# Optimization experiments

Measured on AMD Instinct MI355X. Metric: run time of the kernel, lower is better.

The kernel has to match this reference:

```python
import jax, jax.numpy as jnp
import numpy as np

G, IN_DIM, OUT_DIM = 100000, 256, 128
B, N = 4096, 8192
ALPHA = 0.2          # LeakyReLU negative slope
NEG_INF = -9e15      # same masking constant as the torch module
EPS = 1e-12          # F.normalize eps


def setup_inputs() -> dict:
    key = jax.random.key(0)
    k1, k2, k3, k4, k5, k6, k7 = jax.random.split(key, 7)
    global_feature = jax.random.normal(k1, (G, IN_DIM), dtype=jnp.float32)
    nodes = jax.random.randint(k2, (B,), 0, G, dtype=jnp.int32)
    unique_nodes = jax.random.randint(k3, (N,), 0, G, dtype=jnp.int32)
    mask = jax.random.randint(k4, (B, N), 0, 2, dtype=jnp.int32)
    # ensure every row has at least one neighbor (original always includes self)
    mask = mask.at[:, 0].set(1)
    # xavier_uniform with gain=1.414
    gain = 1.414
    lim_W = gain * np.sqrt(6.0 / (IN_DIM + OUT_DIM))
    W = jax.random.uniform(k5, (IN_DIM, OUT_DIM), jnp.float32, -lim_W, lim_W)
    lim_a = gain * np.sqrt(6.0 / (2 * OUT_DIM + 1))
    a1 = jax.random.uniform(k6, (OUT_DIM,), jnp.float32, -lim_a, lim_a)
    a2 = jax.random.uniform(k7, (OUT_DIM,), jnp.float32, -lim_a, lim_a)
    return {"global_feature": global_feature, "nodes": nodes,
            "unique_nodes": unique_nodes, "mask": mask,
            "W": W, "a1": a1, "a2": a2}


def reference(global_feature, nodes, unique_nodes, mask, W, a1, a2):
    # project gathered features: [B,F], [N,F]
    h_nodes = global_feature[nodes] @ W
    h_neigh = global_feature[unique_nodes] @ W
    # additive attention scores; equivalent to cat([h_i,h_j]) @ a
    e = h_nodes @ a1[:, None] + (h_neigh @ a2)[None, :]   # [B,N]
    e = jnp.where(e >= 0, e, ALPHA * e)                    # leaky relu
    e = jnp.where(mask > 0, e, NEG_INF)
    attention = jax.nn.softmax(e, axis=1)                  # [B,N]
    out = attention @ h_neigh                              # [B,F]
    norm = jnp.linalg.norm(out, axis=1, keepdims=True)
    out = out / jnp.maximum(norm, EPS)                     # F.normalize p=2
    return out
```

## Files before the change

### kernel.cpp

```cpp
#include <hip/hip_runtime.h>

#define IN_DIM  256
#define OUT_DIM 128
#define B_ROWS  4096
#define N_COLS  8192
#define ALPHA   0.2f

typedef unsigned short u16;
typedef unsigned int   u32;
typedef __attribute__((ext_vector_type(8))) short short8;
typedef __attribute__((ext_vector_type(4))) float floatx4;

__device__ __forceinline__ float bf2f(u16 v){ return __uint_as_float(((u32)v) << 16); }
__device__ __forceinline__ float bflo(u32 v){ return __uint_as_float(v << 16); }
__device__ __forceinline__ float bfhi(u32 v){ return __uint_as_float(v & 0xffff0000u); }
__device__ __forceinline__ u16 f2bf(float f){
    u32 u = __float_as_uint(f);
    u += 0x7fffu + ((u >> 16) & 1u);
    return (u16)(u >> 16);
}

__global__ __launch_bounds__(256) void k_detect(const u32* __restrict__ g, int* __restrict__ flag){
    __shared__ int votes[256];
    int t = threadIdx.x;
    u32 u = g[t];
    int e = (u >> 7) & 0xFF;
    votes[t] = (e >= 110 && e <= 140) ? 1 : 0;
    __syncthreads();
    for (int s = 128; s > 0; s >>= 1){
        if (t < s) votes[t] += votes[t + s];
        __syncthreads();
    }
    if (t == 0) flag[0] = (votes[0] >= 128) ? 1 : 0;
}

__global__ __launch_bounds__(256) void k_wa(const void* __restrict__ W, const void* __restrict__ a1,
                                            const int* __restrict__ flag, float* __restrict__ Wa1){
    __shared__ float a1s[OUT_DIM];
    int t = threadIdx.x;
    const int isbf = *flag;
    if (t < OUT_DIM) a1s[t] = isbf ? bf2f(((const u16*)a1)[t]) : ((const float*)a1)[t];
    __syncthreads();
    float s = 0.f;
    if (isbf){
        const u32* wr = (const u32*)W + t * (OUT_DIM/2);
#pragma unroll 8
        for (int i = 0; i < OUT_DIM/2; i++){
            u32 g = wr[i];
            s += bflo(g) * a1s[2*i] + bfhi(g) * a1s[2*i+1];
        }
    } else {
        const float* wr = (const float*)W + t * OUT_DIM;
#pragma unroll 8
        for (int c = 0; c < OUT_DIM; c++) s += wr[c] * a1s[c];
    }
    Wa1[t] = s;
}

__global__ __launch_bounds__(128) void k_wb(const void* __restrict__ W, const void* __restrict__ a2,
                                            const int* __restrict__ flag,
                                            u16* __restrict__ WB, float* __restrict__ a2f){
    const int c  = threadIdx.x;
    const int kb = blockIdx.x;
    const int isbf = *flag;
    short8 v;
#pragma unroll
    for (int j = 0; j < 8; j++){
        float w = isbf ? bf2f(((const u16*)W)[(kb*8 + j) * OUT_DIM + c])
                       : ((const float*)W)[(kb*8 + j) * OUT_DIM + c];
        v[j] = (short)f2bf(w);
    }
    ((short8*)WB)[kb * OUT_DIM + c] = v;
    if (kb == 0) a2f[c] = isbf ? bf2f(((const u16*)a2)[c]) : ((const float*)a2)[c];
}

__global__ __launch_bounds__(256) void k_hneigh(const void* __restrict__ gf, const int* __restrict__ uniq,
                                                const u16* __restrict__ WB, const float* __restrict__ a2f,
                                                const int* __restrict__ flag,
                                                u16* __restrict__ hB, float* __restrict__ s_neigh){
    const int n0   = blockIdx.x * 16;
    const int t    = threadIdx.x;
    const int lane = t & 63;
    const int wv   = t >> 6;
    const int q    = lane >> 4;
    const int m    = lane & 15;
    const int isbf = *flag;
    const int jb0  = wv * 2;

    const size_t row = (size_t)uniq[n0 + m];
    const short8* wb8 = (const short8*)WB;

    floatx4 acc0 = {0.f,0.f,0.f,0.f};
    floatx4 acc1 = {0.f,0.f,0.f,0.f};

#pragma unroll
    for (int ks = 0; ks < IN_DIM/32; ks++){
        short8 afrag;
        if (isbf){
            afrag = *(const short8*)((const u16*)gf + row * IN_DIM + ks*32 + q*8);
        } else {
            const float* gp = (const float*)gf + row * IN_DIM + ks*32 + q*8;
            float4 f0 = *(const float4*)gp;
            float4 f1 = *(const float4*)(gp + 4);
            afrag[0] = (short)f2bf(f0.x); afrag[1] = (short)f2bf(f0.y);
            afrag[2] = (short)f2bf(f0.z); afrag[3] = (short)f2bf(f0.w);
            afrag[4] = (short)f2bf(f1.x); afrag[5] = (short)f2bf(f1.y);
            afrag[6] = (short)f2bf(f1.z); afrag[7] = (short)f2bf(f1.w);
        }
        const int kb = ks*4 + q;
        short8 b0 = wb8[kb * OUT_DIM + jb0*16 + m];
        short8 b1 = wb8[kb * OUT_DIM + (jb0+1)*16 + m];
        acc0 = __builtin_amdgcn_mfma_f32_16x16x32_bf16(afrag, b0, acc0, 0, 0, 0);
        acc1 = __builtin_amdgcn_mfma_f32_16x16x32_bf16(afrag, b1, acc1, 0, 0, 0);
    }

    {
        u32 lo0 = (u32)f2bf(acc0[0]) | ((u32)f2bf(acc0[1]) << 16);
        u32 hi0 = (u32)f2bf(acc0[2]) | ((u32)f2bf(acc0[3]) << 16);
        u32 lo1 = (u32)f2bf(acc1[0]) | ((u32)f2bf(acc1[1]) << 16);
        u32 hi1 = (u32)f2bf(acc1[2]) | ((u32)f2bf(acc1[3]) << 16);
        uint2 v0; v0.x = lo0; v0.y = hi0;
        uint2 v1; v1.x = lo1; v1.y = hi1;
        u16* base = hB + (size_t)(n0/8 + (q>>1)) * 1024 + (q&1)*4;
        *(uint2*)(base + (jb0*16 + m) * 8)     = v0;
        *(uint2*)(base + ((jb0+1)*16 + m) * 8) = v1;
    }

    __shared__ float sred[4][16];
    float a2c0 = a2f[jb0*16 + m], a2c1 = a2f[(jb0+1)*16 + m];
#pragma unroll
    for (int reg = 0; reg < 4; reg++){
        float pr = acc0[reg]*a2c0 + acc1[reg]*a2c1;
        pr += __shfl_xor(pr, 1); pr += __shfl_xor(pr, 2);
        pr += __shfl_xor(pr, 4); pr += __shfl_xor(pr, 8);
        if (m == 0) sred[wv][q*4 + reg] = pr;
    }
    __syncthreads();
    if (t < 16) s_neigh[n0 + t] = sred[0][t] + sred[1][t] + sred[2][t] + sred[3][t];
}

__global__ __launch_bounds__(256) void k_snode(const void* __restrict__ gf, const int* __restrict__ nodes,
                                               const float* __restrict__ Wa1, const int* __restrict__ flag,
                                               float* __restrict__ s_node){
    int lane = threadIdx.x & 63, wv = threadIdx.x >> 6;
    int b = blockIdx.x * 4 + wv;
    const int isbf = *flag;
    float4 wa = ((const float4*)Wa1)[lane];
    float x0, x1, x2, x3;
    if (isbf){
        uint2 gg = ((const uint2*)((const u16*)gf + (size_t)nodes[b] * IN_DIM))[lane];
        x0 = bflo(gg.x); x1 = bfhi(gg.x); x2 = bflo(gg.y); x3 = bfhi(gg.y);
    } else {
        float4 gg = ((const float4*)((const float*)gf + (size_t)nodes[b] * IN_DIM))[lane];
        x0 = gg.x; x1 = gg.y; x2 = gg.z; x3 = gg.w;
    }
    float s = x0*wa.x + x1*wa.y + x2*wa.z + x3*wa.w;
    for (int off = 32; off > 0; off >>= 1) s += __shfl_down(s, off);
    if (lane == 0) s_node[b] = s;
}

__global__ __launch_bounds__(512, 2) void k_attn(const int* __restrict__ mask,
                                                 const float* __restrict__ s_node,
                                                 const float* __restrict__ s_neigh,
                                                 const u16* __restrict__ hB,
                                                 const int* __restrict__ flag,
                                                 void* __restrict__ out){
    const int b0   = blockIdx.x * 16;
    const int t    = threadIdx.x;
    const int lane = t & 63;
    const int wv   = t >> 6;
    const int q    = lane >> 4;
    const int m    = lane & 15;

    const int n0   = wv * (N_COLS/8);
    const int KS   = (N_COLS/8) / 32;

    floatx4 acc[8];
#pragma unroll
    for (int jb = 0; jb < 8; jb++){ floatx4 z = {0.f,0.f,0.f,0.f}; acc[jb] = z; }

    const float sn = s_node[b0 + m];
    const int rowoff = (b0 + m) * N_COLS;
    const short8* hb8 = (const short8*)hB;

    for (int ks = 0; ks < KS; ks++){
        const int nb = n0 + ks*32 + q*8;
        int4   ma = *(const int4*)  (mask    + rowoff + nb);
        int4   mb = *(const int4*)  (mask    + rowoff + nb + 4);
        float4 sa = *(const float4*)(s_neigh + nb);
        float4 sb = *(const float4*)(s_neigh + nb + 4);

        float e[8] = { sn+sa.x, sn+sa.y, sn+sa.z, sn+sa.w,
                       sn+sb.x, sn+sb.y, sn+sb.z, sn+sb.w };
        int mk[8] = { ma.x, ma.y, ma.z, ma.w, mb.x, mb.y, mb.z, mb.w };
        short8 afrag;
#pragma unroll
        for (int j = 0; j < 8; j++){
            float ee = fmaxf(e[j], ALPHA*e[j]);
            ee = fminf(ee, 60.f);
            float p = mk[j] > 0 ? __expf(ee) : 0.f;
            afrag[j] = (short)f2bf(p);
        }

        const int kb = ((n0 + ks*32) >> 3) + q;
#pragma unroll
        for (int jb = 0; jb < 8; jb++){
            short8 bfr = hb8[kb * OUT_DIM + jb*16 + m];
            acc[jb] = __builtin_amdgcn_mfma_f32_16x16x32_bf16(afrag, bfr, acc[jb], 0, 0, 0);
        }
    }

    __shared__ float red[8][16][128];
#pragma unroll
    for (int jb = 0; jb < 8; jb++)
#pragma unroll
        for (int reg = 0; reg < 4; reg++)
            red[wv][q*4 + reg][jb*16 + m] = acc[jb][reg];
    __syncthreads();

    const int c  = t & 127;
    const int rp = t >> 7;
    const int half = (t >> 6) & 1;

    float v[4];
#pragma unroll
    for (int i = 0; i < 4; i++){
        const int r = rp*4 + i;
        float s = 0.f;
#pragma unroll
        for (int w = 0; w < 8; w++) s += red[w][r][c];
        v[i] = s;
    }

    __shared__ float rs[16][2];
#pragma unroll
    for (int i = 0; i < 4; i++){
        float p = v[i] * v[i];
        p += __shfl_xor(p, 1);  p += __shfl_xor(p, 2);  p += __shfl_xor(p, 4);
        p += __shfl_xor(p, 8);  p += __shfl_xor(p, 16); p += __shfl_xor(p, 32);
        if (lane == 0) rs[rp*4 + i][half] = p;
    }
    __syncthreads();

    const int isbf = *flag;
#pragma unroll
    for (int i = 0; i < 4; i++){
        const int r = rp*4 + i;
        float tot = rs[r][0] + rs[r][1];
        float scale = 1.f / fmaxf(sqrtf(tot), 1e-12f);
        float o = v[i] * scale;
        size_t idx = (size_t)(b0 + r) * OUT_DIM + c;
        if (isbf) ((u16*)out)[idx] = f2bf(o);
        else      ((float*)out)[idx] = o;
    }
}

extern "C" void kernel_launch(void* const* d_in, const int* in_sizes, int n_in,
                              void* d_out, int out_size, void* d_ws, size_t ws_size,
                              hipStream_t stream){
    const void* gf    = d_in[0];
    const int*  nodes = (const int*)d_in[1];
    const int*  uniq  = (const int*)d_in[2];
    const int*  mask  = (const int*)d_in[3];
    const void* W     = d_in[4];
    const void* a1    = d_in[5];
    const void* a2    = d_in[6];

    char* ws = (char*)d_ws;
    u16*   hB      = (u16*)ws;
    u16*   WB      = (u16*)(ws + (2u<<20));
    float* s_neigh = (float*)(ws + (2u<<20) + (64u<<10));
    float* s_node  = (float*)(ws + (2u<<20) + (96u<<10));
    float* Wa1     = (float*)(ws + (2u<<20) + (112u<<10));
    float* a2f     = (float*)(ws + (2u<<20) + (113u<<10));
    int*   flag    = (int*)  (ws + (2u<<20) + (114u<<10));

    hipLaunchKernelGGL(k_detect, dim3(1),           dim3(256), 0, stream, (const u32*)gf, flag);
    hipLaunchKernelGGL(k_wa,     dim3(1),           dim3(256), 0, stream, W, a1, flag, Wa1);
    hipLaunchKernelGGL(k_wb,     dim3(32),          dim3(128), 0, stream, W, a2, flag, WB, a2f);
    hipLaunchKernelGGL(k_snode,  dim3(B_ROWS/4),    dim3(256), 0, stream, gf, nodes, Wa1, flag, s_node);
    hipLaunchKernelGGL(k_hneigh, dim3(N_COLS/16),   dim3(256), 0, stream, gf, uniq, WB, a2f, flag, hB, s_neigh);
    hipLaunchKernelGGL(k_attn,   dim3(B_ROWS/16),   dim3(512), 0, stream, mask, s_node, s_neigh, hB, flag, d_out);
}
```

Baseline: 314.7 us.

## Restructure attention into split-N tiles with 32-row reuse and fused prep

Merges the dtype-detect, Wa1, W-repack and node-score kernels into fewer launches, with each wave detecting dtype through ballots. The attention kernel now handles 32 rows per block, so each hB fragment feeds two MFMAs. It splits N across four blocks so the grid grows from 256 to 512 blocks. Probabilities are staged through LDS so mask loads are coalesced along N. Partial sums are merged with LDS atomics, written to a workspace and reduced in a separate normalize kernel, which adds an extra pass and a launch.

```diff
diff --git a/kernel.cpp b/kernel.cpp
--- a/kernel.cpp
+++ b/kernel.cpp
@@ -5,6 +5,7 @@
 #define B_ROWS  4096
 #define N_COLS  8192
 #define ALPHA   0.2f
+#define NSP     4
 
 typedef unsigned short u16;
 typedef unsigned int   u32;
@@ -20,63 +21,51 @@
     return (u16)(u >> 16);
 }
 
-__global__ __launch_bounds__(256) void k_detect(const u32* __restrict__ g, int* __restrict__ flag){
-    __shared__ int votes[256];
-    int t = threadIdx.x;
-    u32 u = g[t];
-    int e = (u >> 7) & 0xFF;
-    votes[t] = (e >= 110 && e <= 140) ? 1 : 0;
-    __syncthreads();
-    for (int s = 128; s > 0; s >>= 1){
-        if (t < s) votes[t] += votes[t + s];
-        __syncthreads();
-    }
-    if (t == 0) flag[0] = (votes[0] >= 128) ? 1 : 0;
-}
-
-__global__ __launch_bounds__(256) void k_wa(const void* __restrict__ W, const void* __restrict__ a1,
-                                            const int* __restrict__ flag, float* __restrict__ Wa1){
-    __shared__ float a1s[OUT_DIM];
-    int t = threadIdx.x;
-    const int isbf = *flag;
-    if (t < OUT_DIM) a1s[t] = isbf ? bf2f(((const u16*)a1)[t]) : ((const float*)a1)[t];
-    __syncthreads();
-    float s = 0.f;
-    if (isbf){
-        const u32* wr = (const u32*)W + t * (OUT_DIM/2);
-#pragma unroll 8
-        for (int i = 0; i < OUT_DIM/2; i++){
-            u32 g = wr[i];
-            s += bflo(g) * a1s[2*i] + bfhi(g) * a1s[2*i+1];
-        }
-    } else {
-        const float* wr = (const float*)W + t * OUT_DIM;
-#pragma unroll 8
-        for (int c = 0; c < OUT_DIM; c++) s += wr[c] * a1s[c];
-    }
-    Wa1[t] = s;
-}
-
-__global__ __launch_bounds__(128) void k_wb(const void* __restrict__ W, const void* __restrict__ a2,
-                                            const int* __restrict__ flag,
-                                            u16* __restrict__ WB, float* __restrict__ a2f){
+__device__ __forceinline__ int detect_bf16_wave(const u32* __restrict__ g){
+    int lane = threadIdx.x & 63;
+    uint4 u = ((const uint4*)g)[lane];
+#define CHK(x) ((((x) >> 7) & 0xFF) >= 110 && (((x) >> 7) & 0xFF) <= 140)
+    unsigned long long c0 = __ballot(CHK(u.x)), c1 = __ballot(CHK(u.y));
+    unsigned long long c2 = __ballot(CHK(u.z)), c3 = __ballot(CHK(u.w));
+#undef CHK
+    int votes = __popcll(c0) + __popcll(c1) + __popcll(c2) + __popcll(c3);
+    return votes >= 128;
+}
+
+__global__ __launch_bounds__(128) void k_prep(const void* __restrict__ gf,
+                                              const void* __restrict__ W, const void* __restrict__ a1,
+                                              const void* __restrict__ a2,
+                                              u16* __restrict__ WB, float* __restrict__ Wa1,
+                                              float* __restrict__ a2f){
+    const int isbf = detect_bf16_wave((const u32*)gf);
     const int c  = threadIdx.x;
     const int kb = blockIdx.x;
-    const int isbf = *flag;
-    short8 v;
+    float a1c = isbf ? bf2f(((const u16*)a1)[c]) : ((const float*)a1)[c];
+    float w[8]; short8 v;
 #pragma unroll
     for (int j = 0; j < 8; j++){
-        float w = isbf ? bf2f(((const u16*)W)[(kb*8 + j) * OUT_DIM + c])
-                       : ((const float*)W)[(kb*8 + j) * OUT_DIM + c];
-        v[j] = (short)f2bf(w);
+        w[j] = isbf ? bf2f(((const u16*)W)[(kb*8 + j) * OUT_DIM + c])
+                    : ((const float*)W)[(kb*8 + j) * OUT_DIM + c];
+        v[j] = (short)f2bf(w[j]);
     }
     ((short8*)WB)[kb * OUT_DIM + c] = v;
+
+    __shared__ float red[2][8];
+    int lane = c & 63, wv = c >> 6;
+#pragma unroll
+    for (int j = 0; j < 8; j++){
+        float p = w[j] * a1c;
+        p += __shfl_xor(p, 1);  p += __shfl_xor(p, 2);  p += __shfl_xor(p, 4);
+        p += __shfl_xor(p, 8);  p += __shfl_xor(p, 16); p += __shfl_xor(p, 32);
+        if (lane == 0) red[wv][j] = p;
+    }
+    __syncthreads();
+    if (c < 8) Wa1[kb*8 + c] = red[0][c] + red[1][c];
     if (kb == 0) a2f[c] = isbf ? bf2f(((const u16*)a2)[c]) : ((const float*)a2)[c];
 }
 
 __global__ __launch_bounds__(256) void k_hneigh(const void* __restrict__ gf, const int* __restrict__ uniq,
                                                 const u16* __restrict__ WB, const float* __restrict__ a2f,
-                                                const int* __restrict__ flag,
                                                 u16* __restrict__ hB, float* __restrict__ s_neigh){
     const int n0   = blockIdx.x * 16;
     const int t    = threadIdx.x;
@@ -84,7 +73,7 @@
     const int wv   = t >> 6;
     const int q    = lane >> 4;
     const int m    = lane & 15;
-    const int isbf = *flag;
+    const int isbf = detect_bf16_wave((const u32*)gf);
     const int jb0  = wv * 2;
 
     const size_t row = (size_t)uniq[n0 + m];
@@ -139,120 +128,132 @@
     if (t < 16) s_neigh[n0 + t] = sred[0][t] + sred[1][t] + sred[2][t] + sred[3][t];
 }
 
-__global__ __launch_bounds__(256) void k_snode(const void* __restrict__ gf, const int* __restrict__ nodes,
-                                               const float* __restrict__ Wa1, const int* __restrict__ flag,
-                                               float* __restrict__ s_node){
-    int lane = threadIdx.x & 63, wv = threadIdx.x >> 6;
-    int b = blockIdx.x * 4 + wv;
-    const int isbf = *flag;
-    float4 wa = ((const float4*)Wa1)[lane];
-    float x0, x1, x2, x3;
-    if (isbf){
-        uint2 gg = ((const uint2*)((const u16*)gf + (size_t)nodes[b] * IN_DIM))[lane];
-        x0 = bflo(gg.x); x1 = bfhi(gg.x); x2 = bflo(gg.y); x3 = bfhi(gg.y);
-    } else {
-        float4 gg = ((const float4*)((const float*)gf + (size_t)nodes[b] * IN_DIM))[lane];
-        x0 = gg.x; x1 = gg.y; x2 = gg.z; x3 = gg.w;
-    }
-    float s = x0*wa.x + x1*wa.y + x2*wa.z + x3*wa.w;
-    for (int off = 32; off > 0; off >>= 1) s += __shfl_down(s, off);
-    if (lane == 0) s_node[b] = s;
-}
-
-__global__ __launch_bounds__(512, 2) void k_attn(const int* __restrict__ mask,
-                                                 const float* __restrict__ s_node,
+__global__ __launch_bounds__(512, 4) void k_attn(const void* __restrict__ gf, const int* __restrict__ nodes,
+                                                 const int* __restrict__ mask,
+                                                 const float* __restrict__ Wa1,
                                                  const float* __restrict__ s_neigh,
                                                  const u16* __restrict__ hB,
-                                                 const int* __restrict__ flag,
-                                                 void* __restrict__ out){
-    const int b0   = blockIdx.x * 16;
-    const int t    = threadIdx.x;
-    const int lane = t & 63;
-    const int wv   = t >> 6;
-    const int q    = lane >> 4;
-    const int m    = lane & 15;
-
-    const int n0   = wv * (N_COLS/8);
-    const int KS   = (N_COLS/8) / 32;
-
-    floatx4 acc[8];
-#pragma unroll
-    for (int jb = 0; jb < 8; jb++){ floatx4 z = {0.f,0.f,0.f,0.f}; acc[jb] = z; }
-
-    const float sn = s_node[b0 + m];
-    const int rowoff = (b0 + m) * N_COLS;
+                                                 float* __restrict__ out_part){
+    const int bid   = blockIdx.x;
+    const int split = bid & (NSP-1);
+    const int b0    = (bid >> 2) * 32;
+    const int t     = threadIdx.x;
+    const int lane  = t & 63;
+    const int wv    = t >> 6;
+    const int q     = lane >> 4;
+    const int m     = lane & 15;
+    const int isbf  = detect_bf16_wave((const u32*)gf);
+
+    __shared__ __align__(16) u16 p_tile[8][32][72];
+    __shared__ float red[32][128];
+    __shared__ float snode[32];
+
+    {
+        float4 z = {0.f,0.f,0.f,0.f};
+        ((float4*)red)[t*2] = z; ((float4*)red)[t*2+1] = z;
+    }
+
+    {
+        float4 wa = ((const float4*)Wa1)[lane];
+#pragma unroll
+        for (int r4 = 0; r4 < 4; r4++){
+            int row = wv*4 + r4;
+            size_t node = (size_t)nodes[b0 + row];
+            float x0, x1, x2, x3;
+            if (isbf){
+                uint2 gg = ((const uint2*)((const u16*)gf + node * IN_DIM))[lane];
+                x0 = bflo(gg.x); x1 = bfhi(gg.x); x2 = bflo(gg.y); x3 = bfhi(gg.y);
+            } else {
+                float4 gg = ((const float4*)((const float*)gf + node * IN_DIM))[lane];
+                x0 = gg.x; x1 = gg.y; x2 = gg.z; x3 = gg.w;
+            }
+            float s = x0*wa.x + x1*wa.y + x2*wa.z + x3*wa.w;
+            s += __shfl_xor(s, 1);  s += __shfl_xor(s, 2);  s += __shfl_xor(s, 4);
+            s += __shfl_xor(s, 8);  s += __shfl_xor(s, 16); s += __shfl_xor(s, 32);
+            if (lane == 0) snode[row] = s;
+        }
+    }
+    __syncthreads();
+
+    floatx4 accA[8], accB[8];
+#pragma unroll
+    for (int jb = 0; jb < 8; jb++){ floatx4 z = {0.f,0.f,0.f,0.f}; accA[jb] = z; accB[jb] = z; }
+
+    const int nwave = split * (N_COLS/NSP) + wv * 256;
     const short8* hb8 = (const short8*)hB;
 
-    for (int ks = 0; ks < KS; ks++){
-        const int nb = n0 + ks*32 + q*8;
-        int4   ma = *(const int4*)  (mask    + rowoff + nb);
-        int4   mb = *(const int4*)  (mask    + rowoff + nb + 4);
-        float4 sa = *(const float4*)(s_neigh + nb);
-        float4 sb = *(const float4*)(s_neigh + nb + 4);
-
-        float e[8] = { sn+sa.x, sn+sa.y, sn+sa.z, sn+sa.w,
-                       sn+sb.x, sn+sb.y, sn+sb.z, sn+sb.w };
-        int mk[8] = { ma.x, ma.y, ma.z, ma.w, mb.x, mb.y, mb.z, mb.w };
-        short8 afrag;
-#pragma unroll
-        for (int j = 0; j < 8; j++){
-            float ee = fmaxf(e[j], ALPHA*e[j]);
-            ee = fminf(ee, 60.f);
-            float p = mk[j] > 0 ? __expf(ee) : 0.f;
-            afrag[j] = (short)f2bf(p);
-        }
-
-        const int kb = ((n0 + ks*32) >> 3) + q;
-#pragma unroll
-        for (int jb = 0; jb < 8; jb++){
-            short8 bfr = hb8[kb * OUT_DIM + jb*16 + m];
-            acc[jb] = __builtin_amdgcn_mfma_f32_16x16x32_bf16(afrag, bfr, acc[jb], 0, 0, 0);
-        }
-    }
-
-    __shared__ float red[8][16][128];
+    for (int ch = 0; ch < 4; ch++){
+        const int nbase = nwave + ch*64;
+        int4 mk[8];
+#pragma unroll
+        for (int i = 0; i < 8; i++)
+            mk[i] = *(const int4*)(mask + (size_t)(b0 + i*4 + q) * N_COLS + nbase + m*4);
+        float4 sg = *(const float4*)(s_neigh + nbase + m*4);
+
+#pragma unroll
+        for (int i = 0; i < 8; i++){
+            float sn = snode[i*4 + q];
+            float e0 = sn + sg.x, e1 = sn + sg.y, e2 = sn + sg.z, e3 = sn + sg.w;
+            e0 = fmaxf(e0, ALPHA*e0); e1 = fmaxf(e1, ALPHA*e1);
+            e2 = fmaxf(e2, ALPHA*e2); e3 = fmaxf(e3, ALPHA*e3);
+            e0 = fminf(e0, 60.f); e1 = fminf(e1, 60.f);
+            e2 = fminf(e2, 60.f); e3 = fminf(e3, 60.f);
+            float p0 = mk[i].x > 0 ? __expf(e0) : 0.f;
+            float p1 = mk[i].y > 0 ? __expf(e1) : 0.f;
+            float p2 = mk[i].z > 0 ? __expf(e2) : 0.f;
+            float p3 = mk[i].w > 0 ? __expf(e3) : 0.f;
+            uint2 pv;
+            pv.x = (u32)f2bf(p0) | ((u32)f2bf(p1) << 16);
+            pv.y = (u32)f2bf(p2) | ((u32)f2bf(p3) << 16);
+            *(uint2*)&p_tile[wv][i*4 + q][m*4] = pv;
+        }
+#pragma unroll
+        for (int ks = 0; ks < 2; ks++){
+            short8 aA = *(const short8*)&p_tile[wv][m]     [ks*32 + q*8];
+            short8 aB = *(const short8*)&p_tile[wv][16 + m][ks*32 + q*8];
+            const int kb = ((nbase + ks*32) >> 3) + q;
+#pragma unroll
+            for (int jb = 0; jb < 8; jb++){
+                short8 bfr = hb8[kb * OUT_DIM + jb*16 + m];
+                accA[jb] = __builtin_amdgcn_mfma_f32_16x16x32_bf16(aA, bfr, accA[jb], 0, 0, 0);
+                accB[jb] = __builtin_amdgcn_mfma_f32_16x16x32_bf16(aB, bfr, accB[jb], 0, 0, 0);
+            }
+        }
+    }
+
 #pragma unroll
     for (int jb = 0; jb < 8; jb++)
 #pragma unroll
-        for (int reg = 0; reg < 4; reg++)
-            red[wv][q*4 + reg][jb*16 + m] = acc[jb][reg];
-    __syncthreads();
-
-    const int c  = t & 127;
-    const int rp = t >> 7;
-    const int half = (t >> 6) & 1;
-
-    float v[4];
-#pragma unroll
-    for (int i = 0; i < 4; i++){
-        const int r = rp*4 + i;
-        float s = 0.f;
-#pragma unroll
-        for (int w = 0; w < 8; w++) s += red[w][r][c];
-        v[i] = s;
-    }
-
-    __shared__ float rs[16][2];
-#pragma unroll
-    for (int i = 0; i < 4; i++){
-        float p = v[i] * v[i];
-        p += __shfl_xor(p, 1);  p += __shfl_xor(p, 2);  p += __shfl_xor(p, 4);
-        p += __shfl_xor(p, 8);  p += __shfl_xor(p, 16); p += __shfl_xor(p, 32);
-        if (lane == 0) rs[rp*4 + i][half] = p;
-    }
-    __syncthreads();
-
-    const int isbf = *flag;
-#pragma unroll
-    for (int i = 0; i < 4; i++){
-        const int r = rp*4 + i;
-        float tot = rs[r][0] + rs[r][1];
-        float scale = 1.f / fmaxf(sqrtf(tot), 1e-12f);
-        float o = v[i] * scale;
-        size_t idx = (size_t)(b0 + r) * OUT_DIM + c;
-        if (isbf) ((u16*)out)[idx] = f2bf(o);
-        else      ((float*)out)[idx] = o;
-    }
+        for (int reg = 0; reg < 4; reg++){
+            atomicAdd(&red[q*4 + reg][jb*16 + m],      accA[jb][reg]);
+            atomicAdd(&red[16 + q*4 + reg][jb*16 + m], accB[jb][reg]);
+        }
+    __syncthreads();
+
+    float* op = out_part + ((size_t)split * B_ROWS + b0) * OUT_DIM;
+    ((float4*)op)[t*2]   = ((float4*)red)[t*2];
+    ((float4*)op)[t*2+1] = ((float4*)red)[t*2+1];
+}
+
+__global__ __launch_bounds__(128) void k_norm(const float* __restrict__ out_part,
+                                              const void* __restrict__ gf, void* __restrict__ out){
+    const int isbf = detect_bf16_wave((const u32*)gf);
+    const int b = blockIdx.x, c = threadIdx.x;
+    float v = 0.f;
+#pragma unroll
+    for (int s = 0; s < NSP; s++)
+        v += out_part[((size_t)s * B_ROWS + b) * OUT_DIM + c];
+    float ss = v * v;
+    for (int off = 32; off > 0; off >>= 1) ss += __shfl_down(ss, off);
+    __shared__ float red[2];
+    int lane = c & 63, wv = c >> 6;
+    if (lane == 0) red[wv] = ss;
+    __syncthreads();
+    float tot = red[0] + red[1];
+    float scale = 1.f / fmaxf(sqrtf(tot), 1e-12f);
+    float o = v * scale;
+    if (isbf) ((u16*)out)[(size_t)b * OUT_DIM + c] = f2bf(o);
+    else      ((float*)out)[(size_t)b * OUT_DIM + c] = o;
 }
 
 extern "C" void kernel_launch(void* const* d_in, const int* in_sizes, int n_in,
@@ -267,18 +268,15 @@
     const void* a2    = d_in[6];
 
     char* ws = (char*)d_ws;
-    u16*   hB      = (u16*)ws;
-    u16*   WB      = (u16*)(ws + (2u<<20));
-    float* s_neigh = (float*)(ws + (2u<<20) + (64u<<10));
-    float* s_node  = (float*)(ws + (2u<<20) + (96u<<10));
-    float* Wa1     = (float*)(ws + (2u<<20) + (112u<<10));
-    float* a2f     = (float*)(ws + (2u<<20) + (113u<<10));
-    int*   flag    = (int*)  (ws + (2u<<20) + (114u<<10));
-
-    hipLaunchKernelGGL(k_detect, dim3(1),           dim3(256), 0, stream, (const u32*)gf, flag);
-    hipLaunchKernelGGL(k_wa,     dim3(1),           dim3(256), 0, stream, W, a1, flag, Wa1);
-    hipLaunchKernelGGL(k_wb,     dim3(32),          dim3(128), 0, stream, W, a2, flag, WB, a2f);
-    hipLaunchKernelGGL(k_snode,  dim3(B_ROWS/4),    dim3(256), 0, stream, gf, nodes, Wa1, flag, s_node);
-    hipLaunchKernelGGL(k_hneigh, dim3(N_COLS/16),   dim3(256), 0, stream, gf, uniq, WB, a2f, flag, hB, s_neigh);
-    hipLaunchKernelGGL(k_attn,   dim3(B_ROWS/16),   dim3(512), 0, stream, mask, s_node, s_neigh, hB, flag, d_out);
-}
+    u16*   hB       = (u16*)ws;
+    u16*   WB       = (u16*)(ws + (2u<<20));
+    float* s_neigh  = (float*)(ws + (2u<<20) + (64u<<10));
+    float* Wa1      = (float*)(ws + (2u<<20) + (96u<<10));
+    float* a2f      = (float*)(ws + (2u<<20) + (97u<<10));
+    float* out_part = (float*)(ws + (2u<<20) + (128u<<10));
+
+    hipLaunchKernelGGL(k_prep,   dim3(32),          dim3(128), 0, stream, gf, W, a1, a2, WB, Wa1, a2f);
+    hipLaunchKernelGGL(k_hneigh, dim3(N_COLS/16),   dim3(256), 0, stream, gf, uniq, WB, a2f, hB, s_neigh);
+    hipLaunchKernelGGL(k_attn,   dim3((B_ROWS/32)*NSP), dim3(512), 0, stream, gf, nodes, mask, Wa1, s_neigh, hB, out_part);
+    hipLaunchKernelGGL(k_norm,   dim3(B_ROWS),      dim3(128), 0, stream, out_part, gf, d_out);
+}
```

Measured after the change: 364.3 us. 15.8% more time.
